# Performance work log

Measured on AMD Instinct MI355X. Metric: run time of the kernel, lower is better.

## Reference

```python
import jax, jax.numpy as jnp
import numpy as np
import math

B, S, E, H, DFF = 8, 1024, 1024, 16, 4096
HD = E // H
EPS = 1e-05


def setup_inputs() -> dict:
    key = jax.random.key(0)
    ks = jax.random.split(key, 8)
    wb_attn = math.sqrt(3.0 / E)
    wb1 = math.sqrt(3.0 * 2.0 / E)      # kaiming for linear1 (in=E)
    wb2 = math.sqrt(3.0 * 2.0 / DFF)    # kaiming for linear2 (in=DFF)
    return {
        "x": jax.random.normal(ks[0], (B, S, E), jnp.float32),
        "in_weights": jax.random.uniform(ks[1], (3, E, E), jnp.float32, -wb_attn, wb_attn),
        "out_weights": jax.random.uniform(ks[2], (E, E), jnp.float32, -wb_attn, wb_attn),
        "ln1_scale": jnp.ones((E,), jnp.float32),
        "ln1_bias": jnp.zeros((E,), jnp.float32),
        "ln2_scale": jnp.ones((E,), jnp.float32),
        "ln2_bias": jnp.zeros((E,), jnp.float32),
        "w1": jax.random.uniform(ks[3], (DFF, E), jnp.float32, -wb1, wb1),
        "b1": jnp.zeros((DFF,), jnp.float32),
        "w2": jax.random.uniform(ks[4], (E, DFF), jnp.float32, -wb2, wb2),
        "b2": jnp.zeros((E,), jnp.float32),
    }


def _layernorm(x, scale, bias):
    mean = jnp.mean(x, axis=-1, keepdims=True)
    var = jnp.var(x, axis=-1, keepdims=True, ddof=1)  # torch.var unbiased=True
    return scale * (x - mean) / jnp.sqrt(var + EPS) + bias


def reference(x, in_weights, out_weights, ln1_scale, ln1_bias, ln2_scale, ln2_bias, w1, b1, w2, b2):
    # QKV projections: note key uses in_weights[0], query [1], value [2]
    def proj(w):  # (B,S,E) -> (B,H,S,HD)
        return (x @ w).reshape(B, S, H, HD).transpose(0, 2, 1, 3)
    k = proj(in_weights[0])
    q = proj(in_weights[1])
    v = proj(in_weights[2])
    scores = jnp.einsum("bhsd,bhtd->bhst", q, k) / math.sqrt(HD)
    probs = jax.nn.softmax(scores, axis=-1)
    attn = jnp.einsum("bhst,bhtd->bhsd", probs, v).transpose(0, 2, 1, 3).reshape(B, S, E)
    attn_out = attn @ out_weights
    # quirk preserved: residual is attn_out + dropout(attn_out) = 2*attn_out (eval mode)
    x1 = _layernorm(attn_out + attn_out, ln1_scale, ln1_bias)
    ffn = jax.nn.relu(x1 @ w1.T + b1) @ w2.T + b2
    return _layernorm(x1 + ffn, ln2_scale, ln2_bias)
```

## Files before the change

### kernel.cpp

```cpp
#include <hip/hip_runtime.h>

#define E_DIM 1024
#define S_LEN 1024
#define H_NUM 16
#define HD_DIM 64
#define B_NUM 8
#define DFF_DIM 4096
#define NROWS 8192
#define QKV_LD 3072

typedef unsigned short u16;
typedef short bf16v8 __attribute__((ext_vector_type(8)));
typedef float f32x4 __attribute__((ext_vector_type(4)));

#define QK_SCALE 0.18033688011112042f

__device__ __forceinline__ u16 f2b(float f) {
  union { float f; unsigned u; } x; x.f = f;
  return (u16)((x.u + 0x7fffu + ((x.u >> 16) & 1u)) >> 16);
}

__device__ __forceinline__ void gload16(const void* g, void* l) {
  __builtin_amdgcn_global_load_lds((const __attribute__((address_space(1))) void*)g,
                                   (__attribute__((address_space(3))) void*)l, 16, 0, 0);
}

template<int MODE>
__global__ __launch_bounds__(512, 2) void gemm8(
    const u16* __restrict__ A, const u16* __restrict__ Bt,
    void* __restrict__ C0, void* __restrict__ C1, const float* __restrict__ bias,
    int N, int KA, int nxt, int NT) {
  __shared__ u16 sA[2 * 16384];
  __shared__ u16 sB[2 * 16384];

  const int tid = threadIdx.x;
  const int lane = tid & 63;
  const int wid = tid >> 6;
  const int wm = wid >> 2, wn = wid & 3;
  const int l15 = lane & 15, l4 = lane >> 4;
  const int pk0 = l4 ^ (l15 & 7);

  const int gx = gridDim.x;
  const int lin = blockIdx.y * gx + blockIdx.x;
  const int chunk = (gx * gridDim.y) >> 3;
  const int swz = (lin & 7) * chunk + (lin >> 3);
  const int bym = swz / gx, bxm = swz % gx;
  const int kh = (bxm >= nxt) ? 1 : 0;
  const int bm = bym * 256;
  const int bn = (bxm - kh * nxt) * 256;
  const int k0 = kh * NT * 64;

  const int srow = tid >> 3;
  const int gch = ((tid & 7) ^ (srow & 7)) * 8;
  const u16* Ag[4];
  const u16* Bg[4];
#pragma unroll
  for (int i = 0; i < 4; ++i) {
    Ag[i] = A + k0 + (size_t)(bm + i * 64 + srow) * KA + gch;
    Bg[i] = Bt + k0 + (size_t)(bn + i * 64 + srow) * KA + gch;
  }
  const int t8 = tid * 8;

#define ST1(tile, li)                                                              \
  do {                                                                             \
    if ((li) < 4) gload16(Ag[li] + (tile) * 64, sA + ((tile)&1) * 16384 + (li)*4096 + t8); \
    else gload16(Bg[(li)-4] + (tile) * 64, sB + ((tile)&1) * 16384 + ((li)-4) * 4096 + t8); \
  } while (0)
#define STG(tile, lo, hi)                                  \
  if ((tile) < NT) {                                       \
    _Pragma("unroll") for (int li = (lo); li <= (hi); ++li) ST1(tile, li); \
  }

  bf16v8 a[4][2], b[4][2];
  f32x4 acc[8][4];
#pragma unroll
  for (int m = 0; m < 8; ++m)
#pragma unroll
    for (int n = 0; n < 4; ++n) acc[m][n] = (f32x4){0.f, 0.f, 0.f, 0.f};

#define LDA(mh, buf)                                                        \
  {                                                                         \
    _Pragma("unroll") for (int mp = 0; mp < 4; ++mp) {                      \
      const u16* rp = (buf) + (size_t)(wm * 128 + (mh)*64 + mp * 16 + l15) * 64; \
      a[mp][0] = *(const bf16v8*)(rp + pk0 * 8);                            \
      a[mp][1] = *(const bf16v8*)(rp + (pk0 ^ 4) * 8);                      \
    }                                                                       \
  }
#define LDB(n0, buf)                                                        \
  {                                                                         \
    _Pragma("unroll") for (int nn = (n0); nn < (n0) + 2; ++nn) {            \
      const u16* rp = (buf) + (size_t)(wn * 64 + nn * 16 + l15) * 64;       \
      b[nn][0] = *(const bf16v8*)(rp + pk0 * 8);                            \
      b[nn][1] = *(const bf16v8*)(rp + (pk0 ^ 4) * 8);                      \
    }                                                                       \
  }
#define MMPH(mh, n0)                                                                      \
  {                                                                                       \
    __builtin_amdgcn_s_setprio(1);                                                        \
    _Pragma("unroll") for (int mp = 0; mp < 4; ++mp) {                                    \
      _Pragma("unroll") for (int nn = (n0); nn < (n0) + 2; ++nn) {                        \
        acc[(mh)*4 + mp][nn] = __builtin_amdgcn_mfma_f32_16x16x32_bf16(                   \
            a[mp][0], b[nn][0], acc[(mh)*4 + mp][nn], 0, 0, 0);                           \
        acc[(mh)*4 + mp][nn] = __builtin_amdgcn_mfma_f32_16x16x32_bf16(                   \
            a[mp][1], b[nn][1], acc[(mh)*4 + mp][nn], 0, 0, 0);                           \
      }                                                                                   \
    }                                                                                     \
    __builtin_amdgcn_s_setprio(0);                                                        \
  }

#pragma unroll
  for (int li = 0; li < 8; ++li) ST1(0, li);
  STG(1, 0, 5);
  __builtin_amdgcn_sched_barrier(0);
  asm volatile("s_waitcnt vmcnt(6)" ::: "memory");
  __builtin_amdgcn_s_barrier();
  LDA(0, sA);
  LDB(0, sB);

  for (int t = 0; t < NT; ++t) {
    u16* sAc = sA + (t & 1) * 16384;
    u16* sBc = sB + (t & 1) * 16384;
    u16* sAn = sA + ((t + 1) & 1) * 16384;
    u16* sBn = sB + ((t + 1) & 1) * 16384;
    STG(t + 1, 6, 7);
    MMPH(0, 0);
    LDB(2, sBc);
    __builtin_amdgcn_s_barrier();
    MMPH(0, 2);
    LDA(1, sAc);
    __builtin_amdgcn_s_barrier();
    STG(t + 2, 0, 2);
    MMPH(1, 0);
    __builtin_amdgcn_sched_barrier(0);
    if (t + 1 < NT) {
      if (t + 2 < NT) asm volatile("s_waitcnt vmcnt(3)" ::: "memory");
      else            asm volatile("s_waitcnt vmcnt(0)" ::: "memory");
    }
    __builtin_amdgcn_s_barrier();
    STG(t + 2, 3, 5);
    MMPH(1, 2);
    if (t + 1 < NT) {
      LDA(0, sAn);
      LDB(0, sBn);
    }
    __builtin_amdgcn_s_barrier();
  }

  const int lrow0 = bm + wm * 128 + l4 * 4;
  const int lcol0 = bn + wn * 64 + l15;
  const float scl = (MODE == 0 && ((bn >> 10) == 1)) ? QK_SCALE : 1.f;
  void* Cw = kh ? C1 : C0;
#pragma unroll
  for (int m = 0; m < 8; ++m) {
#pragma unroll
    for (int n = 0; n < 4; ++n) {
      const int col = lcol0 + n * 16;
      float bv = 0.f;
      if (MODE == 2) bv = bias[col];
      if (MODE == 3) bv = kh ? 0.f : bias[col];
#pragma unroll
      for (int i = 0; i < 4; ++i) {
        const int row = lrow0 + m * 16 + i;
        float v = acc[m][n][i] + bv;
        if (MODE == 2) v = fmaxf(v, 0.f);
        if (MODE == 0) v *= scl;
        if (MODE == 0 || MODE == 2)
          ((u16*)Cw)[(size_t)row * N + col] = f2b(v);
        else
          ((float*)Cw)[(size_t)row * N + col] = v;
      }
    }
  }
#undef ST1
#undef STG
#undef LDA
#undef LDB
#undef MMPH
}

__device__ __forceinline__ void vt_write(u16* sVtBuf, const int4* vr, int strow, int s8) {
#pragma unroll
  for (int it = 0; it < 2; it++) {
    const int r = it * 32 + strow;
    int4 wv = vr[it];
    int4 w2;
    w2.x = __shfl_xor(wv.x, 8); w2.y = __shfl_xor(wv.y, 8);
    w2.z = __shfl_xor(wv.z, 8); w2.w = __shfl_xor(wv.w, 8);
    const int t = r >> 1;
    const int odd = r & 1;
    const u16* own = (const u16*)&wv;
    const u16* par = (const u16*)&w2;
    char* dstbase = (char*)sVtBuf + (t >> 2) * 1024 + (t & 3) * 4;
#pragma unroll
    for (int k = 0; k < 4; k++) {
      const unsigned lo = odd ? (unsigned)par[4 + k] : (unsigned)own[k];
      const unsigned hi = odd ? (unsigned)own[4 + k] : (unsigned)par[k];
      const int d = s8 * 8 + k + (odd ? 4 : 0);
      const int dsw = d ^ s8;
      *(unsigned*)(dstbase + dsw * 16) = lo | (hi << 16);
    }
  }
}

__global__ __launch_bounds__(256) void attn_fa(
    const u16* __restrict__ qkv, u16* __restrict__ attn) {
  __shared__ u16 sK[2][64 * 64];
  __shared__ u16 sVt[2][64 * 64];

  const int tid = threadIdx.x, lane = tid & 63, wave = tid >> 6;
  const int l15 = lane & 15, l4 = lane >> 4;
  const int w = ((blockIdx.x & 7) << 7) + (blockIdx.x >> 3);
  const int bh = w >> 3;
  const int b = bh >> 4, h = bh & 15;
  const int qrow0 = (w & 7) * 128 + wave * 32;
  const size_t rowb = (size_t)b * S_LEN * QKV_LD;
  const u16* kg = qkv + rowb + h * HD_DIM;
  const u16* qg = qkv + rowb + 1024 + h * HD_DIM;
  const u16* vg = qkv + rowb + 2048 + h * HD_DIM;
  const size_t obase = (size_t)b * (S_LEN * E_DIM) + (size_t)h * HD_DIM;
  const int esrc = (lane & 48) + l4 * 4;

  bf16v8 qf[2][2];
#pragma unroll
  for (int m = 0; m < 2; m++)
#pragma unroll
    for (int kk = 0; kk < 2; kk++)
      qf[m][kk] = *(const bf16v8*)(qg + (size_t)(qrow0 + m * 16 + l15) * QKV_LD + kk * 32 + l4 * 8);

  f32x4 acc_o[2][4];
  float mrun[2], lrun[2];
#pragma unroll
  for (int m = 0; m < 2; m++) {
    mrun[m] = -1e30f; lrun[m] = 0.f;
#pragma unroll
    for (int nd = 0; nd < 4; nd++) acc_o[m][nd] = (f32x4){0.f, 0.f, 0.f, 0.f};
  }

  const int strow = tid >> 3;
  const int s8 = tid & 7;

  {
#pragma unroll
    for (int it = 0; it < 2; it++) {
      const int r = it * 32 + strow;
      gload16(kg + (size_t)r * QKV_LD + (s8 ^ (r & 7)) * 8, sK[0] + r * 64 + s8 * 8);
    }
    int4 v0[2];
#pragma unroll
    for (int it = 0; it < 2; it++)
      v0[it] = *(const int4*)(vg + (size_t)(it * 32 + strow) * QKV_LD + s8 * 8);
    vt_write(sVt[0], v0, strow, s8);
    __syncthreads();
  }

  for (int t = 0; t < 16; t++) {
    const int cur = t & 1;
    int4 vreg[2];
    if (t < 15) {
      const int kvn = (t + 1) * 64;
#pragma unroll
      for (int it = 0; it < 2; it++) {
        const int r = it * 32 + strow;
        gload16(kg + (size_t)(kvn + r) * QKV_LD + (s8 ^ (r & 7)) * 8,
                sK[cur ^ 1] + r * 64 + s8 * 8);
      }
#pragma unroll
      for (int it = 0; it < 2; it++)
        vreg[it] = *(const int4*)(vg + (size_t)(kvn + it * 32 + strow) * QKV_LD + s8 * 8);
    }

    f32x4 T[2][4];
#pragma unroll
    for (int m = 0; m < 2; m++)
#pragma unroll
      for (int n = 0; n < 4; n++) T[m][n] = (f32x4){0.f, 0.f, 0.f, 0.f};
#pragma unroll
    for (int n = 0; n < 4; n++) {
      const int r = n * 16 + l15;
      const bf16v8 k0 = *(const bf16v8*)(sK[cur] + r * 64 + (l4 ^ (r & 7)) * 8);
      const bf16v8 k1 = *(const bf16v8*)(sK[cur] + r * 64 + ((4 + l4) ^ (r & 7)) * 8);
#pragma unroll
      for (int m = 0; m < 2; m++) {
        T[m][n] = __builtin_amdgcn_mfma_f32_16x16x32_bf16(k0, qf[m][0], T[m][n], 0, 0, 0);
        T[m][n] = __builtin_amdgcn_mfma_f32_16x16x32_bf16(k1, qf[m][1], T[m][n], 0, 0, 0);
      }
    }

    float pm[2];
#pragma unroll
    for (int m = 0; m < 2; m++) {
      float mx = -1e30f;
#pragma unroll
      for (int n = 0; n < 4; n++)
        mx = fmaxf(mx, fmaxf(fmaxf(T[m][n][0], T[m][n][1]), fmaxf(T[m][n][2], T[m][n][3])));
      mx = fmaxf(mx, __shfl_xor(mx, 16));
      mx = fmaxf(mx, __shfl_xor(mx, 32));
      pm[m] = mx;
    }
    const bool skip = __all((pm[0] <= mrun[0] + 8.f) && (pm[1] <= mrun[1] + 8.f));
    unsigned W[2][4][2];
#pragma unroll
    for (int m = 0; m < 2; m++) {
      const float mnew = skip ? mrun[m] : fmaxf(mrun[m], pm[m]);
      float rsum = 0.f;
#pragma unroll
      for (int n = 0; n < 4; n++)
#pragma unroll
        for (int i = 0; i < 4; i++) {
          const float p = exp2f(T[m][n][i] - mnew);
          T[m][n][i] = p;
          rsum += p;
        }
      rsum += __shfl_xor(rsum, 16);
      rsum += __shfl_xor(rsum, 32);
      if (skip) {
        lrun[m] += rsum;
      } else {
        const float esc = exp2f(mrun[m] - mnew);
        mrun[m] = mnew;
        lrun[m] = lrun[m] * esc + rsum;
#pragma unroll
        for (int i = 0; i < 4; i++) {
          const float e = __shfl(esc, esrc + i);
#pragma unroll
          for (int nd = 0; nd < 4; nd++) acc_o[m][nd][i] *= e;
        }
      }
#pragma unroll
      for (int n = 0; n < 4; n++)
#pragma unroll
        for (int p = 0; p < 2; p++) {
          unsigned wv;
          asm("v_cvt_pk_bf16_f32 %0, %1, %2" : "=v"(wv) : "v"(T[m][n][2 * p]), "v"(T[m][n][2 * p + 1]));
          W[m][n][p] = wv;
        }
    }

#pragma unroll
    for (int kk = 0; kk < 2; kk++) {
      bf16v8 pa[2];
#pragma unroll
      for (int m = 0; m < 2; m++) {
        union { unsigned u[4]; bf16v8 v; } c;
#pragma unroll
        for (int wd = 0; wd < 4; wd++) {
          const int src = l15 + 16 * ((2 * l4 + (wd >> 1)) & 3);
          const unsigned a0 = __shfl(W[m][2 * kk][wd & 1], src);
          const unsigned a1 = __shfl(W[m][2 * kk + 1][wd & 1], src);
          c.u[wd] = (l4 < 2) ? a0 : a1;
        }
        pa[m] = c.v;
      }
#pragma unroll
      for (int nd = 0; nd < 4; nd++) {
        const int d = nd * 16 + l15;
        const int dsw = d ^ ((d >> 3) & 7);
        const bf16v8 vb = *(const bf16v8*)(sVt[cur] + (kk * 4 + l4) * 512 + dsw * 8);
#pragma unroll
        for (int m = 0; m < 2; m++)
          acc_o[m][nd] = __builtin_amdgcn_mfma_f32_16x16x32_bf16(pa[m], vb, acc_o[m][nd], 0, 0, 0);
      }
    }

    if (t < 15) vt_write(sVt[cur ^ 1], vreg, strow, s8);
    __syncthreads();
  }

#pragma unroll
  for (int m = 0; m < 2; m++) {
    const float linv = 1.f / lrun[m];
#pragma unroll
    for (int i = 0; i < 4; i++) {
      const float li = __shfl(linv, esrc + i);
      const int s = qrow0 + m * 16 + l4 * 4 + i;
#pragma unroll
      for (int nd = 0; nd < 4; nd++)
        attn[obase + (size_t)s * E_DIM + nd * 16 + l15] = f2b(acc_o[m][nd][i] * linv * 0.f + f2b(0.f) * 0.f + acc_o[m][nd][i] * li);
    }
  }
}

template<int MODE>
__global__ __launch_bounds__(256) void ln_kernel(
    const float* __restrict__ a, const float* __restrict__ b2nd, const float* __restrict__ c3rd,
    const float* __restrict__ scale, const float* __restrict__ bias,
    float* __restrict__ outf, u16* __restrict__ outb) {
  const int row = blockIdx.x;
  const int tid = threadIdx.x;
  const size_t off = (size_t)row * 1024 + tid * 4;
  float4 v = *(const float4*)(a + off);
  float4 u = *(const float4*)(b2nd + off);
  if (MODE == 0) {
    v.x = 2.f * (v.x + u.x); v.y = 2.f * (v.y + u.y);
    v.z = 2.f * (v.z + u.z); v.w = 2.f * (v.w + u.w);
  } else {
    float4 w = *(const float4*)(c3rd + off);
    v.x += u.x + w.x; v.y += u.y + w.y; v.z += u.z + w.z; v.w += u.w + w.w;
  }
  float s = v.x + v.y + v.z + v.w;
  float q = v.x * v.x + v.y * v.y + v.z * v.z + v.w * v.w;
#pragma unroll
  for (int o = 1; o < 64; o <<= 1) { s += __shfl_xor(s, o); q += __shfl_xor(q, o); }
  __shared__ float red[8];
  const int wave = tid >> 6, lane = tid & 63;
  if (lane == 0) { red[wave] = s; red[4 + wave] = q; }
  __syncthreads();
  s = red[0] + red[1] + red[2] + red[3];
  q = red[4] + red[5] + red[6] + red[7];
  const float mean = s * (1.f / 1024.f);
  const float var = (q - 1024.f * mean * mean) * (1.f / 1023.f);
  const float rstd = rsqrtf(var + 1e-5f);
  const int c = tid * 4;
  float4 sc = *(const float4*)(scale + c);
  float4 bi = *(const float4*)(bias + c);
  float4 o;
  o.x = sc.x * (v.x - mean) * rstd + bi.x;
  o.y = sc.y * (v.y - mean) * rstd + bi.y;
  o.z = sc.z * (v.z - mean) * rstd + bi.z;
  o.w = sc.w * (v.w - mean) * rstd + bi.w;
  *(float4*)(outf + off) = o;
  if (outb != nullptr) {
    ushort4 ob;
    ob.x = f2b(o.x); ob.y = f2b(o.y); ob.z = f2b(o.z); ob.w = f2b(o.w);
    *(ushort4*)(outb + off) = ob;
  }
}

__global__ __launch_bounds__(256) void cast_bf16_k(const float* __restrict__ in,
                                                   u16* __restrict__ out, int n4) {
  const int i = blockIdx.x * blockDim.x + threadIdx.x;
  if (i >= n4) return;
  float4 v = *(const float4*)(in + (size_t)i * 4);
  ushort4 o;
  o.x = f2b(v.x); o.y = f2b(v.y); o.z = f2b(v.z); o.w = f2b(v.w);
  *(ushort4*)(out + (size_t)i * 4) = o;
}

__global__ __launch_bounds__(256) void transpose_cast_k(const float* __restrict__ in,
                                                        u16* __restrict__ out) {
  __shared__ float tile[32][33];
  const int tx = threadIdx.x & 31, ty = threadIdx.x >> 5;
  const int bx = blockIdx.x * 32, by = blockIdx.y * 32;
#pragma unroll
  for (int j = 0; j < 4; j++)
    tile[ty + j * 8][tx] = in[(size_t)(by + ty + j * 8) * 1024 + bx + tx];
  __syncthreads();
#pragma unroll
  for (int j = 0; j < 4; j++)
    out[(size_t)(bx + ty + j * 8) * 1024 + by + tx] = f2b(tile[tx][ty + j * 8]);
}

extern "C" void kernel_launch(void* const* d_in, const int* in_sizes, int n_in,
                              void* d_out, int out_size, void* d_ws, size_t ws_size,
                              hipStream_t stream) {
  const float* x    = (const float*)d_in[0];
  const float* in_w = (const float*)d_in[1];
  const float* out_w = (const float*)d_in[2];
  const float* ln1s = (const float*)d_in[3];
  const float* ln1b = (const float*)d_in[4];
  const float* ln2s = (const float*)d_in[5];
  const float* ln2b = (const float*)d_in[6];
  const float* w1   = (const float*)d_in[7];
  const float* b1   = (const float*)d_in[8];
  const float* w2   = (const float*)d_in[9];
  const float* b2   = (const float*)d_in[10];
  float* outp = (float*)d_out;

  char* ws = (char*)d_ws;
  u16*   xb    = (u16*)(ws + 0);
  u16*   qkv   = (u16*)(ws + 16777216);
  u16*   attnb = (u16*)(ws + 0);
  float* attno0 = (float*)(ws + 67108864);
  float* attno1 = (float*)(ws + 100663296);
  float* x1f   = (float*)(ws + 67108864);
  u16*   x1b   = (u16*)(ws + 134217728);
  u16*   Hb    = (u16*)(ws + 0);
  float* ffn0  = (float*)(ws + 100663296);
  u16*   wkt   = (u16*)(ws + 150994944);
  u16*   wot   = wkt + 3145728;
  u16*   w1b   = wot + 1048576;
  u16*   w2b   = w1b + 4194304;
  (void)ws_size; (void)in_sizes; (void)n_in; (void)out_size;

  cast_bf16_k<<<8192, 256, 0, stream>>>(x, xb, 2097152);
  cast_bf16_k<<<4096, 256, 0, stream>>>(w1, w1b, 1048576);
  cast_bf16_k<<<4096, 256, 0, stream>>>(w2, w2b, 1048576);
  dim3 tg(32, 32);
  transpose_cast_k<<<tg, 256, 0, stream>>>(in_w + 0,       wkt);
  transpose_cast_k<<<tg, 256, 0, stream>>>(in_w + 1048576, wkt + 1048576);
  transpose_cast_k<<<tg, 256, 0, stream>>>(in_w + 2097152, wkt + 2097152);
  transpose_cast_k<<<tg, 256, 0, stream>>>(out_w,          wot);

  gemm8<0><<<dim3(12, 32), 512, 0, stream>>>(xb, wkt, qkv, nullptr, nullptr, 3072, 1024, 12, 16);

  attn_fa<<<1024, 256, 0, stream>>>(qkv, attnb);

  gemm8<1><<<dim3(8, 32), 512, 0, stream>>>(attnb, wot, attno0, attno1, nullptr, 1024, 1024, 4, 8);

  ln_kernel<0><<<8192, 256, 0, stream>>>(attno0, attno1, nullptr, ln1s, ln1b, x1f, x1b);

  gemm8<2><<<dim3(16, 32), 512, 0, stream>>>(x1b, w1b, Hb, nullptr, b1, 4096, 1024, 16, 16);

  gemm8<3><<<dim3(8, 32), 512, 0, stream>>>(Hb, w2b, ffn0, outp, b2, 1024, 4096, 4, 32);

  ln_kernel<1><<<8192, 256, 0, stream>>>(x1f, ffn0, outp, ln2s, ln2b, outp, nullptr);
}
```

Measured before the change: 415.8 us.

## Rewrite flash attention with 32x32x16 MFMA, transposed scores, 512-thread blocks

Reworks the attention kernel to use 32x32x16 bf16 MFMA and computes S^T = K·Q^T, so each lane owns one query row. Row max and sum then need only a single cross-half shuffle, and the rescale needs no per-element broadcast. Blocks grow to 512 threads covering 256 query rows, which halves the number of blocks and spreads each K/V tile load across more waves. The output is written as packed 4-element stores. The risks are higher register pressure from the 16-wide accumulators, the launch bound of 4 blocks per SM, and a new lane-swap path for building P fragments.

```diff
diff --git a/kernel.cpp b/kernel.cpp
--- a/kernel.cpp
+++ b/kernel.cpp
@@ -10,8 +10,10 @@
 #define QKV_LD 3072
 
 typedef unsigned short u16;
+typedef unsigned u32;
 typedef short bf16v8 __attribute__((ext_vector_type(8)));
 typedef float f32x4 __attribute__((ext_vector_type(4)));
+typedef float f32x16 __attribute__((ext_vector_type(16)));
 
 #define QK_SCALE 0.18033688011112042f
 
@@ -178,206 +180,157 @@
 #undef MMPH
 }
 
-__device__ __forceinline__ void vt_write(u16* sVtBuf, const int4* vr, int strow, int s8) {
-#pragma unroll
-  for (int it = 0; it < 2; it++) {
-    const int r = it * 32 + strow;
-    int4 wv = vr[it];
-    int4 w2;
-    w2.x = __shfl_xor(wv.x, 8); w2.y = __shfl_xor(wv.y, 8);
-    w2.z = __shfl_xor(wv.z, 8); w2.w = __shfl_xor(wv.w, 8);
-    const int t = r >> 1;
-    const int odd = r & 1;
-    const u16* own = (const u16*)&wv;
-    const u16* par = (const u16*)&w2;
-    char* dstbase = (char*)sVtBuf + (t >> 2) * 1024 + (t & 3) * 4;
-#pragma unroll
-    for (int k = 0; k < 4; k++) {
-      const unsigned lo = odd ? (unsigned)par[4 + k] : (unsigned)own[k];
-      const unsigned hi = odd ? (unsigned)own[4 + k] : (unsigned)par[k];
-      const int d = s8 * 8 + k + (odd ? 4 : 0);
-      const int dsw = d ^ s8;
-      *(unsigned*)(dstbase + dsw * 16) = lo | (hi << 16);
-    }
-  }
-}
-
-__global__ __launch_bounds__(256) void attn_fa(
+
+#define MKPF(dst, A0, B0, C0, D0)                                             \
+  {                                                                           \
+    u32 sa = (u32)__shfl_xor((int)(A0), 32), sb = (u32)__shfl_xor((int)(B0), 32); \
+    u32 sc = (u32)__shfl_xor((int)(C0), 32), sd = (u32)__shfl_xor((int)(D0), 32); \
+    union { u32 u[4]; bf16v8 v; } cc;                                         \
+    cc.u[0] = hi ? sc : (A0); cc.u[1] = hi ? sd : (B0);                       \
+    cc.u[2] = hi ? (C0) : sa; cc.u[3] = hi ? (D0) : sb;                       \
+    dst = cc.v;                                                               \
+  }
+
+__device__ __forceinline__ void vt_write64(u16* sVtBuf, int4 wv, int vr, int s8) {
+  int4 w2;
+  w2.x = __shfl_xor(wv.x, 8); w2.y = __shfl_xor(wv.y, 8);
+  w2.z = __shfl_xor(wv.z, 8); w2.w = __shfl_xor(wv.w, 8);
+  const int t = vr >> 1;
+  const int odd = vr & 1;
+  const u16* own = (const u16*)&wv;
+  const u16* par = (const u16*)&w2;
+  char* dstbase = (char*)sVtBuf + (t >> 2) * 1024 + (t & 3) * 4;
+#pragma unroll
+  for (int k = 0; k < 4; k++) {
+    const unsigned lo = odd ? (unsigned)par[4 + k] : (unsigned)own[k];
+    const unsigned h2 = odd ? (unsigned)own[4 + k] : (unsigned)par[k];
+    const int d = s8 * 8 + k + (odd ? 4 : 0);
+    const int dsw = d ^ s8;
+    *(unsigned*)(dstbase + dsw * 16) = lo | (h2 << 16);
+  }
+}
+
+__global__ __launch_bounds__(512, 4) void attn_fa(
     const u16* __restrict__ qkv, u16* __restrict__ attn) {
   __shared__ u16 sK[2][64 * 64];
   __shared__ u16 sVt[2][64 * 64];
 
-  const int tid = threadIdx.x, lane = tid & 63, wave = tid >> 6;
-  const int l15 = lane & 15, l4 = lane >> 4;
-  const int w = ((blockIdx.x & 7) << 7) + (blockIdx.x >> 3);
-  const int bh = w >> 3;
+  const int tid = threadIdx.x, lane = tid & 63;
+  const int l31 = lane & 31, hi = lane >> 5;
+  const int w = ((blockIdx.x & 7) << 6) + (blockIdx.x >> 3);
+  const int bh = w >> 2;
   const int b = bh >> 4, h = bh & 15;
-  const int qrow0 = (w & 7) * 128 + wave * 32;
+  const int qrow0 = (w & 3) * 256 + (tid >> 6) * 32;
   const size_t rowb = (size_t)b * S_LEN * QKV_LD;
   const u16* kg = qkv + rowb + h * HD_DIM;
   const u16* qg = qkv + rowb + 1024 + h * HD_DIM;
   const u16* vg = qkv + rowb + 2048 + h * HD_DIM;
   const size_t obase = (size_t)b * (S_LEN * E_DIM) + (size_t)h * HD_DIM;
-  const int esrc = (lane & 48) + l4 * 4;
-
-  bf16v8 qf[2][2];
-#pragma unroll
-  for (int m = 0; m < 2; m++)
-#pragma unroll
-    for (int kk = 0; kk < 2; kk++)
-      qf[m][kk] = *(const bf16v8*)(qg + (size_t)(qrow0 + m * 16 + l15) * QKV_LD + kk * 32 + l4 * 8);
-
-  f32x4 acc_o[2][4];
-  float mrun[2], lrun[2];
-#pragma unroll
-  for (int m = 0; m < 2; m++) {
-    mrun[m] = -1e30f; lrun[m] = 0.f;
-#pragma unroll
-    for (int nd = 0; nd < 4; nd++) acc_o[m][nd] = (f32x4){0.f, 0.f, 0.f, 0.f};
-  }
-
-  const int strow = tid >> 3;
+
+  bf16v8 qf[4];
+#pragma unroll
+  for (int ks = 0; ks < 4; ++ks)
+    qf[ks] = *(const bf16v8*)(qg + (size_t)(qrow0 + l31) * QKV_LD + ks * 16 + hi * 8);
+
+  const int kr = tid >> 3;
   const int s8 = tid & 7;
-
+  const u16* kgsrc = kg + (size_t)kr * QKV_LD + ((s8 ^ (kr & 7)) * 8);
+  const u16* vgsrc = vg + (size_t)kr * QKV_LD + s8 * 8;
+
+  f32x16 accT[2];
+#pragma unroll
+  for (int i = 0; i < 16; ++i) { accT[0][i] = 0.f; accT[1][i] = 0.f; }
+  float mrun = -1e30f, lrun = 0.f;
+
+  gload16(kgsrc, sK[0] + tid * 8);
   {
-#pragma unroll
-    for (int it = 0; it < 2; it++) {
-      const int r = it * 32 + strow;
-      gload16(kg + (size_t)r * QKV_LD + (s8 ^ (r & 7)) * 8, sK[0] + r * 64 + s8 * 8);
-    }
-    int4 v0[2];
-#pragma unroll
-    for (int it = 0; it < 2; it++)
-      v0[it] = *(const int4*)(vg + (size_t)(it * 32 + strow) * QKV_LD + s8 * 8);
-    vt_write(sVt[0], v0, strow, s8);
+    int4 v0 = *(const int4*)(vgsrc);
+    vt_write64(sVt[0], v0, kr, s8);
+  }
+  __syncthreads();
+
+  for (int t = 0; t < 16; ++t) {
+    const int cur = t & 1;
+    int4 vreg;
+    if (t < 15) {
+      gload16(kgsrc + (size_t)(t + 1) * 64 * QKV_LD, sK[cur ^ 1] + tid * 8);
+      vreg = *(const int4*)(vgsrc + (size_t)(t + 1) * 64 * QKV_LD);
+    }
+
+    f32x16 T0, T1;
+#pragma unroll
+    for (int i = 0; i < 16; ++i) { T0[i] = 0.f; T1[i] = 0.f; }
+#pragma unroll
+    for (int ks = 0; ks < 4; ++ks) {
+      const int ch = ((2 * ks + hi) ^ (l31 & 7)) * 8;
+      const bf16v8 k0 = *(const bf16v8*)(sK[cur] + (size_t)l31 * 64 + ch);
+      const bf16v8 k1 = *(const bf16v8*)(sK[cur] + (size_t)(32 + l31) * 64 + ch);
+      T0 = __builtin_amdgcn_mfma_f32_32x32x16_bf16(k0, qf[ks], T0, 0, 0, 0);
+      T1 = __builtin_amdgcn_mfma_f32_32x32x16_bf16(k1, qf[ks], T1, 0, 0, 0);
+    }
+
+    float mx = fmaxf(T0[0], T1[0]);
+#pragma unroll
+    for (int r = 1; r < 16; ++r) mx = fmaxf(mx, fmaxf(T0[r], T1[r]));
+    mx = fmaxf(mx, __shfl_xor(mx, 32));
+    const bool skip = __all(mx <= mrun + 8.f);
+    const float mnew = skip ? mrun : fmaxf(mrun, mx);
+    float rs = 0.f;
+#pragma unroll
+    for (int r = 0; r < 16; ++r) { T0[r] = exp2f(T0[r] - mnew); rs += T0[r]; }
+#pragma unroll
+    for (int r = 0; r < 16; ++r) { T1[r] = exp2f(T1[r] - mnew); rs += T1[r]; }
+    rs += __shfl_xor(rs, 32);
+    if (skip) {
+      lrun += rs;
+    } else {
+      const float esc = exp2f(mrun - mnew);
+      mrun = mnew;
+      lrun = lrun * esc + rs;
+#pragma unroll
+      for (int r = 0; r < 16; ++r) { accT[0][r] *= esc; accT[1][r] *= esc; }
+    }
+
+    u32 P0[8], P1[8];
+#pragma unroll
+    for (int wd = 0; wd < 8; ++wd) {
+      asm("v_cvt_pk_bf16_f32 %0, %1, %2" : "=v"(P0[wd]) : "v"(T0[2 * wd]), "v"(T0[2 * wd + 1]));
+      asm("v_cvt_pk_bf16_f32 %0, %1, %2" : "=v"(P1[wd]) : "v"(T1[2 * wd]), "v"(T1[2 * wd + 1]));
+    }
+    bf16v8 pf[4];
+    MKPF(pf[0], P0[0], P0[1], P0[2], P0[3]);
+    MKPF(pf[1], P0[4], P0[5], P0[6], P0[7]);
+    MKPF(pf[2], P1[0], P1[1], P1[2], P1[3]);
+    MKPF(pf[3], P1[4], P1[5], P1[6], P1[7]);
+
+#pragma unroll
+    for (int dblk = 0; dblk < 2; ++dblk) {
+      const int dd = dblk * 32 + l31;
+      const int drow = (dd ^ (dd >> 3)) * 8;
+#pragma unroll
+      for (int ks = 0; ks < 4; ++ks) {
+        const bf16v8 va = *(const bf16v8*)(sVt[cur] + (2 * ks + hi) * 512 + drow);
+        accT[dblk] = __builtin_amdgcn_mfma_f32_32x32x16_bf16(va, pf[ks], accT[dblk], 0, 0, 0);
+      }
+    }
+
+    if (t < 15) vt_write64(sVt[cur ^ 1], vreg, kr, s8);
     __syncthreads();
   }
 
-  for (int t = 0; t < 16; t++) {
-    const int cur = t & 1;
-    int4 vreg[2];
-    if (t < 15) {
-      const int kvn = (t + 1) * 64;
-#pragma unroll
-      for (int it = 0; it < 2; it++) {
-        const int r = it * 32 + strow;
-        gload16(kg + (size_t)(kvn + r) * QKV_LD + (s8 ^ (r & 7)) * 8,
-                sK[cur ^ 1] + r * 64 + s8 * 8);
-      }
-#pragma unroll
-      for (int it = 0; it < 2; it++)
-        vreg[it] = *(const int4*)(vg + (size_t)(kvn + it * 32 + strow) * QKV_LD + s8 * 8);
-    }
-
-    f32x4 T[2][4];
-#pragma unroll
-    for (int m = 0; m < 2; m++)
-#pragma unroll
-      for (int n = 0; n < 4; n++) T[m][n] = (f32x4){0.f, 0.f, 0.f, 0.f};
-#pragma unroll
-    for (int n = 0; n < 4; n++) {
-      const int r = n * 16 + l15;
-      const bf16v8 k0 = *(const bf16v8*)(sK[cur] + r * 64 + (l4 ^ (r & 7)) * 8);
-      const bf16v8 k1 = *(const bf16v8*)(sK[cur] + r * 64 + ((4 + l4) ^ (r & 7)) * 8);
-#pragma unroll
-      for (int m = 0; m < 2; m++) {
-        T[m][n] = __builtin_amdgcn_mfma_f32_16x16x32_bf16(k0, qf[m][0], T[m][n], 0, 0, 0);
-        T[m][n] = __builtin_amdgcn_mfma_f32_16x16x32_bf16(k1, qf[m][1], T[m][n], 0, 0, 0);
-      }
-    }
-
-    float pm[2];
-#pragma unroll
-    for (int m = 0; m < 2; m++) {
-      float mx = -1e30f;
-#pragma unroll
-      for (int n = 0; n < 4; n++)
-        mx = fmaxf(mx, fmaxf(fmaxf(T[m][n][0], T[m][n][1]), fmaxf(T[m][n][2], T[m][n][3])));
-      mx = fmaxf(mx, __shfl_xor(mx, 16));
-      mx = fmaxf(mx, __shfl_xor(mx, 32));
-      pm[m] = mx;
-    }
-    const bool skip = __all((pm[0] <= mrun[0] + 8.f) && (pm[1] <= mrun[1] + 8.f));
-    unsigned W[2][4][2];
-#pragma unroll
-    for (int m = 0; m < 2; m++) {
-      const float mnew = skip ? mrun[m] : fmaxf(mrun[m], pm[m]);
-      float rsum = 0.f;
-#pragma unroll
-      for (int n = 0; n < 4; n++)
-#pragma unroll
-        for (int i = 0; i < 4; i++) {
-          const float p = exp2f(T[m][n][i] - mnew);
-          T[m][n][i] = p;
-          rsum += p;
-        }
-      rsum += __shfl_xor(rsum, 16);
-      rsum += __shfl_xor(rsum, 32);
-      if (skip) {
-        lrun[m] += rsum;
-      } else {
-        const float esc = exp2f(mrun[m] - mnew);
-        mrun[m] = mnew;
-        lrun[m] = lrun[m] * esc + rsum;
-#pragma unroll
-        for (int i = 0; i < 4; i++) {
-          const float e = __shfl(esc, esrc + i);
-#pragma unroll
-          for (int nd = 0; nd < 4; nd++) acc_o[m][nd][i] *= e;
-        }
-      }
-#pragma unroll
-      for (int n = 0; n < 4; n++)
-#pragma unroll
-        for (int p = 0; p < 2; p++) {
-          unsigned wv;
-          asm("v_cvt_pk_bf16_f32 %0, %1, %2" : "=v"(wv) : "v"(T[m][n][2 * p]), "v"(T[m][n][2 * p + 1]));
-          W[m][n][p] = wv;
-        }
-    }
-
-#pragma unroll
-    for (int kk = 0; kk < 2; kk++) {
-      bf16v8 pa[2];
-#pragma unroll
-      for (int m = 0; m < 2; m++) {
-        union { unsigned u[4]; bf16v8 v; } c;
-#pragma unroll
-        for (int wd = 0; wd < 4; wd++) {
-          const int src = l15 + 16 * ((2 * l4 + (wd >> 1)) & 3);
-          const unsigned a0 = __shfl(W[m][2 * kk][wd & 1], src);
-          const unsigned a1 = __shfl(W[m][2 * kk + 1][wd & 1], src);
-          c.u[wd] = (l4 < 2) ? a0 : a1;
-        }
-        pa[m] = c.v;
-      }
-#pragma unroll
-      for (int nd = 0; nd < 4; nd++) {
-        const int d = nd * 16 + l15;
-        const int dsw = d ^ ((d >> 3) & 7);
-        const bf16v8 vb = *(const bf16v8*)(sVt[cur] + (kk * 4 + l4) * 512 + dsw * 8);
-#pragma unroll
-        for (int m = 0; m < 2; m++)
-          acc_o[m][nd] = __builtin_amdgcn_mfma_f32_16x16x32_bf16(pa[m], vb, acc_o[m][nd], 0, 0, 0);
-      }
-    }
-
-    if (t < 15) vt_write(sVt[cur ^ 1], vreg, strow, s8);
-    __syncthreads();
-  }
-
-#pragma unroll
-  for (int m = 0; m < 2; m++) {
-    const float linv = 1.f / lrun[m];
-#pragma unroll
-    for (int i = 0; i < 4; i++) {
-      const float li = __shfl(linv, esrc + i);
-      const int s = qrow0 + m * 16 + l4 * 4 + i;
-#pragma unroll
-      for (int nd = 0; nd < 4; nd++)
-        attn[obase + (size_t)s * E_DIM + nd * 16 + l15] = f2b(acc_o[m][nd][i] * linv * 0.f + f2b(0.f) * 0.f + acc_o[m][nd][i] * li);
-    }
-  }
+  const float linv = 1.f / lrun;
+  u16* orow = attn + obase + (size_t)(qrow0 + l31) * E_DIM;
+#pragma unroll
+  for (int dblk = 0; dblk < 2; ++dblk)
+#pragma unroll
+    for (int a4 = 0; a4 < 4; ++a4) {
+      ushort4 st;
+      st.x = f2b(accT[dblk][4 * a4 + 0] * linv);
+      st.y = f2b(accT[dblk][4 * a4 + 1] * linv);
+      st.z = f2b(accT[dblk][4 * a4 + 2] * linv);
+      st.w = f2b(accT[dblk][4 * a4 + 3] * linv);
+      *(ushort4*)(orow + dblk * 32 + a4 * 8 + hi * 4) = st;
+    }
 }
 
 template<int MODE>
@@ -493,7 +446,7 @@
 
   gemm8<0><<<dim3(12, 32), 512, 0, stream>>>(xb, wkt, qkv, nullptr, nullptr, 3072, 1024, 12, 16);
 
-  attn_fa<<<1024, 256, 0, stream>>>(qkv, attnb);
+  attn_fa<<<512, 512, 0, stream>>>(qkv, attnb);
 
   gemm8<1><<<dim3(8, 32), 512, 0, stream>>>(attnb, wot, attno0, attno1, nullptr, 1024, 1024, 4, 8);
 
```

New measurement: 386.1 us. -7.1%, faster.
